# Kernel tuning notes

Measured on AMD Instinct MI355X. Metric: run time of the kernel, lower is better.

Reference implementation:

```python
import jax, jax.numpy as jnp
import numpy as np


def setup_inputs() -> dict:
    key = jax.random.key(0)
    k1, k2, k3 = jax.random.split(key, 3)
    B, N, F = 32, 1024, 128
    x = jax.random.normal(k1, (B, N, F), dtype=jnp.float32)
    adj = jax.random.uniform(k2, (B, N, N), dtype=jnp.float32)
    # Linear(in_feature=128, out_feature=128) params (Kaiming-ish scale)
    W = jax.random.normal(k3, (F, F), dtype=jnp.float32) * (1.0 / np.sqrt(F))
    b = jnp.zeros((F,), dtype=jnp.float32)
    return {"x": x, "adj": adj, "W": W, "b": b}


def reference(x, adj, W, b):
    # h = W(x) ; dropout is identity in inference mode
    h = jnp.einsum("bnf,fg->bng", x, W) + b          # [B,N,F]
    h = jnp.einsum("bnm,bmf->bnf", adj, h)           # neighbor aggregation
    return jax.nn.relu(h + x)                          # residual + ReLU
```

## Files before the change

### kernel.cpp

```cpp
#include <hip/hip_runtime.h>
#include <stdint.h>

typedef unsigned short u16;
typedef __attribute__((ext_vector_type(4))) u16    u16x4;
typedef __attribute__((ext_vector_type(8))) u16    u16x8;
typedef __attribute__((ext_vector_type(4))) float  f32x4;
typedef __attribute__((ext_vector_type(8))) __bf16 bf16x8;

__device__ __forceinline__ u16 f2bf(float f) {
    union { float f; uint32_t u; } v; v.f = f;
    uint32_t u = v.u;
    uint32_t rb = 0x7FFFu + ((u >> 16) & 1u);
    return (u16)((u + rb) >> 16);
}

__global__ __launch_bounds__(256) void gcn_wt(const float* __restrict__ W,
                                              u16* __restrict__ Wt) {
    int idx = blockIdx.x * 256 + threadIdx.x;
    int k = idx >> 7, f = idx & 127;
    Wt[f * 128 + k] = f2bf(W[idx]);
}

__global__ __launch_bounds__(256) void gcn_xw(const float* __restrict__ x,
                                              const u16* __restrict__ Wt,
                                              const float* __restrict__ bias,
                                              u16* __restrict__ hT) {
    __shared__ u16 Wl[128 * 128];
    __shared__ u16 Xl[128 * 128];
    const int t  = threadIdx.x;
    const int bb = blockIdx.x >> 3;
    const int n0 = (blockIdx.x & 7) << 7;

#pragma unroll
    for (int i = 0; i < 16; ++i) {
        int o  = i * 256 + t;
        int f  = o >> 5;
        int kb = (o & 31) * 8;
        u16x4 v = *(const u16x4*)((const char*)Wt + o * 8);
        *(u16x4*)((char*)Wl + f * 256 + (kb ^ ((f & 7) << 4))) = v;
    }
    const float* xb = x + (size_t)bb * (1024 * 128) + (size_t)n0 * 128;
#pragma unroll
    for (int i = 0; i < 16; ++i) {
        int o4 = i * 256 + t;
        int n  = o4 >> 5;
        int kb = (o4 & 31) * 8;
        f32x4 v = *(const f32x4*)(xb + (size_t)o4 * 4);
        u16x4 h; h.x = f2bf(v.x); h.y = f2bf(v.y); h.z = f2bf(v.z); h.w = f2bf(v.w);
        *(u16x4*)((char*)Xl + n * 256 + (kb ^ ((n & 7) << 4))) = h;
    }
    __syncthreads();

    const int w = t >> 6, l = t & 63;
    const int wr = w >> 1, wc = w & 1;
    f32x4 acc[4][4] = {};
#pragma unroll
    for (int kk = 0; kk < 4; ++kk) {
        const int kbyte = kk * 64 + (l >> 4) * 16;
        bf16x8 a[4], b[4];
#pragma unroll
        for (int mf = 0; mf < 4; ++mf) {
            int fl = wr * 64 + mf * 16 + (l & 15);
            a[mf] = *(const bf16x8*)((const char*)Wl + fl * 256 + (kbyte ^ ((fl & 7) << 4)));
        }
#pragma unroll
        for (int nn = 0; nn < 4; ++nn) {
            int nl = wc * 64 + nn * 16 + (l & 15);
            b[nn] = *(const bf16x8*)((const char*)Xl + nl * 256 + (kbyte ^ ((nl & 7) << 4)));
        }
#pragma unroll
        for (int mf = 0; mf < 4; ++mf)
#pragma unroll
            for (int nn = 0; nn < 4; ++nn)
                acc[mf][nn] = __builtin_amdgcn_mfma_f32_16x16x32_bf16(
                    a[mf], b[nn], acc[mf][nn], 0, 0, 0);
    }

    u16* ho = hT + (size_t)bb * 131072;
#pragma unroll
    for (int mf = 0; mf < 4; ++mf) {
        int fbase = wr * 64 + mf * 16 + (l >> 4) * 4;
#pragma unroll
        for (int r = 0; r < 4; ++r) {
            float bv = bias[fbase + r];
#pragma unroll
            for (int nn = 0; nn < 4; ++nn) {
                int n = wc * 64 + nn * 16 + (l & 15);
                ho[(size_t)(fbase + r) * 1024 + n0 + n] = f2bf(acc[mf][nn][r] + bv);
            }
        }
    }
}

__global__ __launch_bounds__(512, 4) void gcn_agg(const float* __restrict__ adj,
                                                  const u16* __restrict__ hT,
                                                  const float* __restrict__ x,
                                                  float* __restrict__ out) {
    __shared__ u16 Al[2][64 * 64];
    __shared__ u16 Bl[2][128 * 64];

    const int t = threadIdx.x;
    const int L  = (blockIdx.x & 7) * 64 + (blockIdx.x >> 3);
    const int bb = L >> 4;
    const int r0 = (L & 15) << 6;

    const float* adjb = adj + (size_t)bb * 1048576 + (size_t)r0 * 1024;
    const u16*   hTb  = hT + (size_t)bb * 131072;

    const int w = t >> 6, l = t & 63;
    const int wr = w >> 1, wc = w & 1;

    const int rA  = t >> 3, k8 = t & 7;
    const float* gA  = adjb + (size_t)rA * 1024 + k8 * 8;
    const u16*   gB0 = hTb + (size_t)rA * 1024 + k8 * 8;
    const u16*   gB1 = gB0 + 64 * 1024;
    const int ldsA  = rA * 128 + ((k8 * 16) ^ ((rA & 7) << 4));
    const int ldsB0 = rA * 128 + ((k8 * 16) ^ ((rA & 7) << 4));
    const int ldsB1 = (64 + rA) * 128 + ((k8 * 16) ^ ((rA & 7) << 4));

#define LOADT(ar, br, ks)                                   \
    do {                                                    \
        const int k0 = (ks) * 64;                           \
        ar[0] = *(const f32x4*)(gA + k0);                   \
        ar[1] = *(const f32x4*)(gA + k0 + 4);               \
        br[0] = *(const u16x8*)(gB0 + k0);                  \
        br[1] = *(const u16x8*)(gB1 + k0);                  \
    } while (0)

#define WRITET(buf, ar, br)                                 \
    do {                                                    \
        u16x8 ha;                                           \
        ha[0] = f2bf(ar[0].x); ha[1] = f2bf(ar[0].y);       \
        ha[2] = f2bf(ar[0].z); ha[3] = f2bf(ar[0].w);       \
        ha[4] = f2bf(ar[1].x); ha[5] = f2bf(ar[1].y);       \
        ha[6] = f2bf(ar[1].z); ha[7] = f2bf(ar[1].w);       \
        *(u16x8*)((char*)&Al[buf][0] + ldsA)  = ha;         \
        *(u16x8*)((char*)&Bl[buf][0] + ldsB0) = br[0];      \
        *(u16x8*)((char*)&Bl[buf][0] + ldsB1) = br[1];      \
    } while (0)

#define BARRIER() asm volatile("s_waitcnt lgkmcnt(0)\ns_barrier" ::: "memory")

#define COMPUTE(buf)                                                            \
    do {                                                                        \
        _Pragma("unroll")                                                       \
        for (int kk = 0; kk < 2; ++kk) {                                        \
            const int kbyte = kk * 64 + (l >> 4) * 16;                          \
            const int rl = wr * 16 + (l & 15);                                  \
            bf16x8 a = *(const bf16x8*)((const char*)&Al[buf][0] + rl * 128 +   \
                                        (kbyte ^ ((rl & 7) << 4)));             \
            bf16x8 b[4];                                                        \
            _Pragma("unroll")                                                   \
            for (int nn = 0; nn < 4; ++nn) {                                    \
                int fl = wc * 64 + nn * 16 + (l & 15);                          \
                b[nn] = *(const bf16x8*)((const char*)&Bl[buf][0] + fl * 128 +  \
                                         (kbyte ^ ((fl & 7) << 4)));            \
            }                                                                   \
            _Pragma("unroll")                                                   \
            for (int nn = 0; nn < 4; ++nn)                                      \
                acc[nn] = __builtin_amdgcn_mfma_f32_16x16x32_bf16(              \
                    a, b[nn], acc[nn], 0, 0, 0);                                \
        }                                                                       \
    } while (0)

    f32x4 acc[4] = {};
    f32x4 a0[2], a1[2];
    u16x8 b0[2], b1[2];

    LOADT(a0, b0, 0);
    LOADT(a1, b1, 1);
#pragma unroll
    for (int ks = 0; ks < 16; ks += 2) {
        WRITET(0, a0, b0);
        BARRIER();
        if (ks + 2 < 16) LOADT(a0, b0, ks + 2);
        COMPUTE(0);
        WRITET(1, a1, b1);
        BARRIER();
        if (ks + 3 < 16) LOADT(a1, b1, ks + 3);
        COMPUTE(1);
    }
#undef LOADT
#undef WRITET
#undef BARRIER
#undef COMPUTE

    const float* xb = x + (size_t)bb * 131072;
    float*       ob = out + (size_t)bb * 131072;
#pragma unroll
    for (int j = 0; j < 4; ++j) {
        int r = r0 + wr * 16 + (l >> 4) * 4 + j;
#pragma unroll
        for (int nn = 0; nn < 4; ++nn) {
            int f = wc * 64 + nn * 16 + (l & 15);
            size_t idx = (size_t)r * 128 + f;
            float v = acc[nn][j] + xb[idx];
            ob[idx] = fmaxf(v, 0.0f);
        }
    }
}

extern "C" void kernel_launch(void* const* d_in, const int* in_sizes, int n_in,
                              void* d_out, int out_size, void* d_ws, size_t ws_size,
                              hipStream_t stream) {
    const float* x    = (const float*)d_in[0];
    const float* adj  = (const float*)d_in[1];
    const float* W    = (const float*)d_in[2];
    const float* bias = (const float*)d_in[3];
    float* out = (float*)d_out;

    u16* hT = (u16*)d_ws;
    u16* Wt = (u16*)((char*)d_ws + (size_t)32 * 131072 * 2);

    gcn_wt <<<dim3(64),  dim3(256), 0, stream>>>(W, Wt);
    gcn_xw <<<dim3(256), dim3(256), 0, stream>>>(x, Wt, bias, hT);
    gcn_agg<<<dim3(512), dim3(512), 0, stream>>>(adj, hT, x, out);
}
```

Measured before the change: 40.89 us.

## Reassociate to (adj·x)·W and fuse both GEMMs into one kernel

Reorders the computation as (adj @ x) @ W, with the bias term handled through adjacency row sums (Rs[r] * bias). This removes the separate x@W kernel and the bf16 hT intermediate that had to be written to and read back from global memory. Each block loads its raw fp32 x tiles, converts them to bf16 and transposes them into padded shared memory. It then multiplies the 64x128 aggregated tile by Wt, read directly from global memory. The cost is more per-block work: a scalar transposed x load pattern, one extra bf16 rounding of the intermediate, and more shared memory per block, which may reduce occupancy.

```diff
diff --git a/kernel.cpp b/kernel.cpp
--- a/kernel.cpp
+++ b/kernel.cpp
@@ -21,83 +21,15 @@
     Wt[f * 128 + k] = f2bf(W[idx]);
 }
 
-__global__ __launch_bounds__(256) void gcn_xw(const float* __restrict__ x,
-                                              const u16* __restrict__ Wt,
-                                              const float* __restrict__ bias,
-                                              u16* __restrict__ hT) {
-    __shared__ u16 Wl[128 * 128];
-    __shared__ u16 Xl[128 * 128];
-    const int t  = threadIdx.x;
-    const int bb = blockIdx.x >> 3;
-    const int n0 = (blockIdx.x & 7) << 7;
-
-#pragma unroll
-    for (int i = 0; i < 16; ++i) {
-        int o  = i * 256 + t;
-        int f  = o >> 5;
-        int kb = (o & 31) * 8;
-        u16x4 v = *(const u16x4*)((const char*)Wt + o * 8);
-        *(u16x4*)((char*)Wl + f * 256 + (kb ^ ((f & 7) << 4))) = v;
-    }
-    const float* xb = x + (size_t)bb * (1024 * 128) + (size_t)n0 * 128;
-#pragma unroll
-    for (int i = 0; i < 16; ++i) {
-        int o4 = i * 256 + t;
-        int n  = o4 >> 5;
-        int kb = (o4 & 31) * 8;
-        f32x4 v = *(const f32x4*)(xb + (size_t)o4 * 4);
-        u16x4 h; h.x = f2bf(v.x); h.y = f2bf(v.y); h.z = f2bf(v.z); h.w = f2bf(v.w);
-        *(u16x4*)((char*)Xl + n * 256 + (kb ^ ((n & 7) << 4))) = h;
-    }
-    __syncthreads();
-
-    const int w = t >> 6, l = t & 63;
-    const int wr = w >> 1, wc = w & 1;
-    f32x4 acc[4][4] = {};
-#pragma unroll
-    for (int kk = 0; kk < 4; ++kk) {
-        const int kbyte = kk * 64 + (l >> 4) * 16;
-        bf16x8 a[4], b[4];
-#pragma unroll
-        for (int mf = 0; mf < 4; ++mf) {
-            int fl = wr * 64 + mf * 16 + (l & 15);
-            a[mf] = *(const bf16x8*)((const char*)Wl + fl * 256 + (kbyte ^ ((fl & 7) << 4)));
-        }
-#pragma unroll
-        for (int nn = 0; nn < 4; ++nn) {
-            int nl = wc * 64 + nn * 16 + (l & 15);
-            b[nn] = *(const bf16x8*)((const char*)Xl + nl * 256 + (kbyte ^ ((nl & 7) << 4)));
-        }
-#pragma unroll
-        for (int mf = 0; mf < 4; ++mf)
-#pragma unroll
-            for (int nn = 0; nn < 4; ++nn)
-                acc[mf][nn] = __builtin_amdgcn_mfma_f32_16x16x32_bf16(
-                    a[mf], b[nn], acc[mf][nn], 0, 0, 0);
-    }
-
-    u16* ho = hT + (size_t)bb * 131072;
-#pragma unroll
-    for (int mf = 0; mf < 4; ++mf) {
-        int fbase = wr * 64 + mf * 16 + (l >> 4) * 4;
-#pragma unroll
-        for (int r = 0; r < 4; ++r) {
-            float bv = bias[fbase + r];
-#pragma unroll
-            for (int nn = 0; nn < 4; ++nn) {
-                int n = wc * 64 + nn * 16 + (l & 15);
-                ho[(size_t)(fbase + r) * 1024 + n0 + n] = f2bf(acc[mf][nn][r] + bv);
-            }
-        }
-    }
-}
-
-__global__ __launch_bounds__(512, 4) void gcn_agg(const float* __restrict__ adj,
-                                                  const u16* __restrict__ hT,
-                                                  const float* __restrict__ x,
-                                                  float* __restrict__ out) {
-    __shared__ u16 Al[2][64 * 64];
-    __shared__ u16 Bl[2][128 * 64];
+__global__ __launch_bounds__(512, 4) void gcn_fused(const float* __restrict__ adj,
+                                                    const float* __restrict__ x,
+                                                    const u16* __restrict__ Wt,
+                                                    const float* __restrict__ bias,
+                                                    float* __restrict__ out) {
+    __shared__ u16   Al[2][64 * 64];
+    __shared__ u16   Xt[2][128 * 72];
+    __shared__ u16   Yl[64 * 128];
+    __shared__ float Rs[64];
 
     const int t = threadIdx.x;
     const int L  = (blockIdx.x & 7) * 64 + (blockIdx.x >> 3);
@@ -105,38 +37,43 @@
     const int r0 = (L & 15) << 6;
 
     const float* adjb = adj + (size_t)bb * 1048576 + (size_t)r0 * 1024;
-    const u16*   hTb  = hT + (size_t)bb * 131072;
+    const float* xb   = x + (size_t)bb * 131072;
 
     const int w = t >> 6, l = t & 63;
     const int wr = w >> 1, wc = w & 1;
 
-    const int rA  = t >> 3, k8 = t & 7;
-    const float* gA  = adjb + (size_t)rA * 1024 + k8 * 8;
-    const u16*   gB0 = hTb + (size_t)rA * 1024 + k8 * 8;
-    const u16*   gB1 = gB0 + 64 * 1024;
-    const int ldsA  = rA * 128 + ((k8 * 16) ^ ((rA & 7) << 4));
-    const int ldsB0 = rA * 128 + ((k8 * 16) ^ ((rA & 7) << 4));
-    const int ldsB1 = (64 + rA) * 128 + ((k8 * 16) ^ ((rA & 7) << 4));
+    const int rA = t >> 3, k8 = t & 7;
+    const float* gA = adjb + (size_t)rA * 1024 + k8 * 8;
+    const int ldsA = rA * 128 + ((k8 * 16) ^ ((rA & 7) << 4));
 
-#define LOADT(ar, br, ks)                                   \
-    do {                                                    \
-        const int k0 = (ks) * 64;                           \
-        ar[0] = *(const f32x4*)(gA + k0);                   \
-        ar[1] = *(const f32x4*)(gA + k0 + 4);               \
-        br[0] = *(const u16x8*)(gB0 + k0);                  \
-        br[1] = *(const u16x8*)(gB1 + k0);                  \
+    const float* gX = xb + (size_t)wr * 128 + wc * 64 + l;
+    const int xWb = (wc * 64 + l) * 144 + 2 * wr;
+
+    float rsum = 0.0f;
+
+#define LOADT(ar, xr, ks)                                       \
+    do {                                                        \
+        const int n0_ = (ks) * 64;                              \
+        ar[0] = *(const f32x4*)(gA + n0_);                      \
+        ar[1] = *(const f32x4*)(gA + n0_ + 4);                  \
+        _Pragma("unroll")                                       \
+        for (int i = 0; i < 16; ++i)                            \
+            xr[i] = gX[(size_t)n0_ * 128 + i * 512];            \
     } while (0)
 
-#define WRITET(buf, ar, br)                                 \
-    do {                                                    \
-        u16x8 ha;                                           \
-        ha[0] = f2bf(ar[0].x); ha[1] = f2bf(ar[0].y);       \
-        ha[2] = f2bf(ar[0].z); ha[3] = f2bf(ar[0].w);       \
-        ha[4] = f2bf(ar[1].x); ha[5] = f2bf(ar[1].y);       \
-        ha[6] = f2bf(ar[1].z); ha[7] = f2bf(ar[1].w);       \
-        *(u16x8*)((char*)&Al[buf][0] + ldsA)  = ha;         \
-        *(u16x8*)((char*)&Bl[buf][0] + ldsB0) = br[0];      \
-        *(u16x8*)((char*)&Bl[buf][0] + ldsB1) = br[1];      \
+#define WRITET(buf, ar, xr)                                     \
+    do {                                                        \
+        u16x8 ha;                                               \
+        ha[0] = f2bf(ar[0].x); ha[1] = f2bf(ar[0].y);           \
+        ha[2] = f2bf(ar[0].z); ha[3] = f2bf(ar[0].w);           \
+        ha[4] = f2bf(ar[1].x); ha[5] = f2bf(ar[1].y);           \
+        ha[6] = f2bf(ar[1].z); ha[7] = f2bf(ar[1].w);           \
+        *(u16x8*)((char*)&Al[buf][0] + ldsA) = ha;              \
+        rsum += ar[0].x + ar[0].y + ar[0].z + ar[0].w           \
+              + ar[1].x + ar[1].y + ar[1].z + ar[1].w;          \
+        _Pragma("unroll")                                       \
+        for (int i = 0; i < 16; ++i)                            \
+            *(u16*)((char*)&Xt[buf][0] + xWb + i * 8) = f2bf(xr[i]); \
     } while (0)
 
 #define BARRIER() asm volatile("s_waitcnt lgkmcnt(0)\ns_barrier" ::: "memory")
@@ -145,16 +82,16 @@
     do {                                                                        \
         _Pragma("unroll")                                                       \
         for (int kk = 0; kk < 2; ++kk) {                                        \
-            const int kbyte = kk * 64 + (l >> 4) * 16;                          \
+            const int kbyteA = kk * 64 + (l >> 4) * 16;                         \
             const int rl = wr * 16 + (l & 15);                                  \
             bf16x8 a = *(const bf16x8*)((const char*)&Al[buf][0] + rl * 128 +   \
-                                        (kbyte ^ ((rl & 7) << 4)));             \
+                                        (kbyteA ^ ((rl & 7) << 4)));            \
             bf16x8 b[4];                                                        \
             _Pragma("unroll")                                                   \
             for (int nn = 0; nn < 4; ++nn) {                                    \
-                int fl = wc * 64 + nn * 16 + (l & 15);                          \
-                b[nn] = *(const bf16x8*)((const char*)&Bl[buf][0] + fl * 128 +  \
-                                         (kbyte ^ ((fl & 7) << 4)));            \
+                int fm = wc * 64 + nn * 16 + (l & 15);                          \
+                b[nn] = *(const bf16x8*)((const char*)&Xt[buf][0] + fm * 144 +  \
+                                         kk * 64 + (l >> 4) * 16);              \
             }                                                                   \
             _Pragma("unroll")                                                   \
             for (int nn = 0; nn < 4; ++nn)                                      \
@@ -165,19 +102,19 @@
 
     f32x4 acc[4] = {};
     f32x4 a0[2], a1[2];
-    u16x8 b0[2], b1[2];
+    float xs0[16], xs1[16];
 
-    LOADT(a0, b0, 0);
-    LOADT(a1, b1, 1);
+    LOADT(a0, xs0, 0);
+    LOADT(a1, xs1, 1);
 #pragma unroll
     for (int ks = 0; ks < 16; ks += 2) {
-        WRITET(0, a0, b0);
+        WRITET(0, a0, xs0);
         BARRIER();
-        if (ks + 2 < 16) LOADT(a0, b0, ks + 2);
+        if (ks + 2 < 16) LOADT(a0, xs0, ks + 2);
         COMPUTE(0);
-        WRITET(1, a1, b1);
+        WRITET(1, a1, xs1);
         BARRIER();
-        if (ks + 3 < 16) LOADT(a1, b1, ks + 3);
+        if (ks + 3 < 16) LOADT(a1, xs1, ks + 3);
         COMPUTE(1);
     }
 #undef LOADT
@@ -185,16 +122,48 @@
 #undef BARRIER
 #undef COMPUTE
 
-    const float* xb = x + (size_t)bb * 131072;
-    float*       ob = out + (size_t)bb * 131072;
+    rsum += __shfl_xor(rsum, 1);
+    rsum += __shfl_xor(rsum, 2);
+    rsum += __shfl_xor(rsum, 4);
+    if ((t & 7) == 0) Rs[rA] = rsum;
+
 #pragma unroll
-    for (int j = 0; j < 4; ++j) {
-        int r = r0 + wr * 16 + (l >> 4) * 4 + j;
+    for (int nn = 0; nn < 4; ++nn)
+#pragma unroll
+        for (int j = 0; j < 4; ++j) {
+            int r = wr * 16 + (l >> 4) * 4 + j;
+            int c = wc * 64 + nn * 16 + (l & 15);
+            *(u16*)((char*)Yl + r * 256 + ((c * 2) ^ ((r & 7) << 4))) =
+                f2bf(acc[nn][j]);
+        }
+    __syncthreads();
+
+    f32x4 z[4] = {};
+    const int rl2 = wr * 16 + (l & 15);
+#pragma unroll
+    for (int kk = 0; kk < 4; ++kk) {
+        const int kbyte = kk * 64 + (l >> 4) * 16;
+        bf16x8 a = *(const bf16x8*)((const char*)Yl + rl2 * 256 +
+                                    (kbyte ^ ((rl2 & 7) << 4)));
 #pragma unroll
         for (int nn = 0; nn < 4; ++nn) {
             int f = wc * 64 + nn * 16 + (l & 15);
-            size_t idx = (size_t)r * 128 + f;
-            float v = acc[nn][j] + xb[idx];
+            int k = kk * 32 + (l >> 4) * 8;
+            bf16x8 b = *(const bf16x8*)(Wt + (size_t)f * 128 + k);
+            z[nn] = __builtin_amdgcn_mfma_f32_16x16x32_bf16(a, b, z[nn], 0, 0, 0);
+        }
+    }
+
+    float* ob = out + (size_t)bb * 131072;
+#pragma unroll
+    for (int nn = 0; nn < 4; ++nn) {
+        int f = wc * 64 + nn * 16 + (l & 15);
+        float bv = bias[f];
+#pragma unroll
+        for (int j = 0; j < 4; ++j) {
+            int r = wr * 16 + (l >> 4) * 4 + j;
+            size_t idx = (size_t)(r0 + r) * 128 + f;
+            float v = z[nn][j] + Rs[r] * bv + xb[idx];
             ob[idx] = fmaxf(v, 0.0f);
         }
     }
@@ -209,10 +178,8 @@
     const float* bias = (const float*)d_in[3];
     float* out = (float*)d_out;
 
-    u16* hT = (u16*)d_ws;
-    u16* Wt = (u16*)((char*)d_ws + (size_t)32 * 131072 * 2);
+    u16* Wt = (u16*)d_ws;
 
-    gcn_wt <<<dim3(64),  dim3(256), 0, stream>>>(W, Wt);
-    gcn_xw <<<dim3(256), dim3(256), 0, stream>>>(x, Wt, bias, hT);
-    gcn_agg<<<dim3(512), dim3(512), 0, stream>>>(adj, hT, x, out);
+    gcn_wt   <<<dim3(64),  dim3(256), 0, stream>>>(W, Wt);
+    gcn_fused<<<dim3(512), dim3(512), 0, stream>>>(adj, x, Wt, bias, out);
 }
```

After: 49.71 us. 21.6% more time.

## Load hT operand straight into registers, drop its LDS staging in aggregation

Applied to the files above, without the earlier changes.

The aggregation kernel now has each wave own 16 feature columns and read its hT B-fragments directly from global memory into registers, so the B tile no longer goes through shared memory. Only the adj tile is staged in LDS, with one barrier per k-step instead of the previous paired double-buffer pattern. The goal is to cut LDS traffic, LDS footprint and write-then-read latency. The cost is more global loads of hT, since each wave fetches its own slice, and B is now prefetched only one step ahead.

```diff
diff --git a/kernel.cpp b/kernel.cpp
--- a/kernel.cpp
+++ b/kernel.cpp
@@ -6,6 +6,8 @@
 typedef __attribute__((ext_vector_type(8))) u16    u16x8;
 typedef __attribute__((ext_vector_type(4))) float  f32x4;
 typedef __attribute__((ext_vector_type(8))) __bf16 bf16x8;
+
+union BF8 { u16x8 u; bf16x8 b; };
 
 __device__ __forceinline__ u16 f2bf(float f) {
     union { float f; uint32_t u; } v; v.f = f;
@@ -97,7 +99,6 @@
                                                   const float* __restrict__ x,
                                                   float* __restrict__ out) {
     __shared__ u16 Al[2][64 * 64];
-    __shared__ u16 Bl[2][128 * 64];
 
     const int t = threadIdx.x;
     const int L  = (blockIdx.x & 7) * 64 + (blockIdx.x >> 3);
@@ -108,96 +109,91 @@
     const u16*   hTb  = hT + (size_t)bb * 131072;
 
     const int w = t >> 6, l = t & 63;
-    const int wr = w >> 1, wc = w & 1;
-
-    const int rA  = t >> 3, k8 = t & 7;
-    const float* gA  = adjb + (size_t)rA * 1024 + k8 * 8;
-    const u16*   gB0 = hTb + (size_t)rA * 1024 + k8 * 8;
-    const u16*   gB1 = gB0 + 64 * 1024;
-    const int ldsA  = rA * 128 + ((k8 * 16) ^ ((rA & 7) << 4));
-    const int ldsB0 = rA * 128 + ((k8 * 16) ^ ((rA & 7) << 4));
-    const int ldsB1 = (64 + rA) * 128 + ((k8 * 16) ^ ((rA & 7) << 4));
-
-#define LOADT(ar, br, ks)                                   \
-    do {                                                    \
-        const int k0 = (ks) * 64;                           \
-        ar[0] = *(const f32x4*)(gA + k0);                   \
-        ar[1] = *(const f32x4*)(gA + k0 + 4);               \
-        br[0] = *(const u16x8*)(gB0 + k0);                  \
-        br[1] = *(const u16x8*)(gB1 + k0);                  \
-    } while (0)
-
-#define WRITET(buf, ar, br)                                 \
-    do {                                                    \
-        u16x8 ha;                                           \
-        ha[0] = f2bf(ar[0].x); ha[1] = f2bf(ar[0].y);       \
-        ha[2] = f2bf(ar[0].z); ha[3] = f2bf(ar[0].w);       \
-        ha[4] = f2bf(ar[1].x); ha[5] = f2bf(ar[1].y);       \
-        ha[6] = f2bf(ar[1].z); ha[7] = f2bf(ar[1].w);       \
-        *(u16x8*)((char*)&Al[buf][0] + ldsA)  = ha;         \
-        *(u16x8*)((char*)&Bl[buf][0] + ldsB0) = br[0];      \
-        *(u16x8*)((char*)&Bl[buf][0] + ldsB1) = br[1];      \
+    const int lc = l & 15, lg = l >> 4;
+    const int f = w * 16 + lc;
+
+    const int rA = t >> 3, k8 = t & 7;
+    const float* gA = adjb + (size_t)rA * 1024 + k8 * 8;
+    const int ldsA = rA * 128 + ((k8 * 16) ^ ((rA & 7) << 4));
+
+    const u16* gB = hTb + (size_t)f * 1024 + lg * 8;
+
+#define LOADA(ar, ks)                                 \
+    do {                                              \
+        ar[0] = *(const f32x4*)(gA + (ks) * 64);      \
+        ar[1] = *(const f32x4*)(gA + (ks) * 64 + 4);  \
+    } while (0)
+
+#define LOADB(br, ks)                                          \
+    do {                                                       \
+        br[0] = *(const u16x8*)(gB + (ks) * 64);               \
+        br[1] = *(const u16x8*)(gB + (ks) * 64 + 32);          \
+    } while (0)
+
+#define WRITEA(buf, ar)                                 \
+    do {                                                \
+        u16x8 ha;                                       \
+        ha[0] = f2bf(ar[0].x); ha[1] = f2bf(ar[0].y);   \
+        ha[2] = f2bf(ar[0].z); ha[3] = f2bf(ar[0].w);   \
+        ha[4] = f2bf(ar[1].x); ha[5] = f2bf(ar[1].y);   \
+        ha[6] = f2bf(ar[1].z); ha[7] = f2bf(ar[1].w);   \
+        *(u16x8*)((char*)&Al[buf][0] + ldsA) = ha;      \
     } while (0)
 
 #define BARRIER() asm volatile("s_waitcnt lgkmcnt(0)\ns_barrier" ::: "memory")
 
-#define COMPUTE(buf)                                                            \
+#define COMPUTE(buf, br)                                                        \
     do {                                                                        \
         _Pragma("unroll")                                                       \
-        for (int kk = 0; kk < 2; ++kk) {                                        \
-            const int kbyte = kk * 64 + (l >> 4) * 16;                          \
-            const int rl = wr * 16 + (l & 15);                                  \
-            bf16x8 a = *(const bf16x8*)((const char*)&Al[buf][0] + rl * 128 +   \
-                                        (kbyte ^ ((rl & 7) << 4)));             \
-            bf16x8 b[4];                                                        \
+        for (int kn = 0; kn < 2; ++kn) {                                        \
+            BF8 bu; bu.u = br[kn];                                              \
             _Pragma("unroll")                                                   \
-            for (int nn = 0; nn < 4; ++nn) {                                    \
-                int fl = wc * 64 + nn * 16 + (l & 15);                          \
-                b[nn] = *(const bf16x8*)((const char*)&Bl[buf][0] + fl * 128 +  \
-                                         (kbyte ^ ((fl & 7) << 4)));            \
+            for (int rb = 0; rb < 4; ++rb) {                                    \
+                int r = rb * 16 + lc;                                           \
+                bf16x8 a = *(const bf16x8*)((const char*)&Al[buf][0] + r * 128  \
+                               + ((kn * 64 + lg * 16) ^ ((r & 7) << 4)));       \
+                yacc[rb] = __builtin_amdgcn_mfma_f32_16x16x32_bf16(             \
+                    a, bu.b, yacc[rb], 0, 0, 0);                                \
             }                                                                   \
-            _Pragma("unroll")                                                   \
-            for (int nn = 0; nn < 4; ++nn)                                      \
-                acc[nn] = __builtin_amdgcn_mfma_f32_16x16x32_bf16(              \
-                    a, b[nn], acc[nn], 0, 0, 0);                                \
         }                                                                       \
     } while (0)
 
-    f32x4 acc[4] = {};
-    f32x4 a0[2], a1[2];
-    u16x8 b0[2], b1[2];
-
-    LOADT(a0, b0, 0);
-    LOADT(a1, b1, 1);
-#pragma unroll
-    for (int ks = 0; ks < 16; ks += 2) {
-        WRITET(0, a0, b0);
+    f32x4 yacc[4] = {};
+    f32x4 aCur[2], aNxt[2];
+    u16x8 bCur[2], bNxt[2];
+
+    LOADA(aCur, 0);
+    LOADB(bCur, 0);
+#pragma unroll
+    for (int ks = 0; ks < 16; ++ks) {
+        const int buf = ks & 1;
+        WRITEA(buf, aCur);
         BARRIER();
-        if (ks + 2 < 16) LOADT(a0, b0, ks + 2);
-        COMPUTE(0);
-        WRITET(1, a1, b1);
-        BARRIER();
-        if (ks + 3 < 16) LOADT(a1, b1, ks + 3);
-        COMPUTE(1);
-    }
-#undef LOADT
-#undef WRITET
+        if (ks + 1 < 16) {
+            LOADA(aNxt, ks + 1);
+            LOADB(bNxt, ks + 1);
+        }
+        COMPUTE(buf, bCur);
+        aCur[0] = aNxt[0]; aCur[1] = aNxt[1];
+        bCur[0] = bNxt[0]; bCur[1] = bNxt[1];
+    }
+#undef LOADA
+#undef LOADB
+#undef WRITEA
 #undef BARRIER
 #undef COMPUTE
 
-    const float* xb = x + (size_t)bb * 131072;
-    float*       ob = out + (size_t)bb * 131072;
-#pragma unroll
-    for (int j = 0; j < 4; ++j) {
-        int r = r0 + wr * 16 + (l >> 4) * 4 + j;
-#pragma unroll
-        for (int nn = 0; nn < 4; ++nn) {
-            int f = wc * 64 + nn * 16 + (l & 15);
-            size_t idx = (size_t)r * 128 + f;
-            float v = acc[nn][j] + xb[idx];
+    const float* xb = x + (size_t)bb * 131072 + (size_t)r0 * 128;
+    float*       ob = out + (size_t)bb * 131072 + (size_t)r0 * 128;
+#pragma unroll
+    for (int rb = 0; rb < 4; ++rb)
+#pragma unroll
+        for (int j = 0; j < 4; ++j) {
+            int rr = rb * 16 + lg * 4 + j;
+            size_t idx = (size_t)rr * 128 + f;
+            float v = yacc[rb][j] + xb[idx];
             ob[idx] = fmaxf(v, 0.0f);
         }
-    }
 }
 
 extern "C" void kernel_launch(void* const* d_in, const int* in_sizes, int n_in,
```

New measurement: 44.81 us. 1.1x slower.
